# Optimization experiments

Hardware: AMD Instinct MI355X
Metric: run time of the kernel (lower is better)

The kernel has to match this reference:

```python
import jax, jax.numpy as jnp
import numpy as np
import math

B, N, ND, ED, CD, H = 4, 128, 256, 128, 256, 8
D = ND // H

def _ln(x):
    m = jnp.mean(x, axis=-1, keepdims=True)
    v = jnp.mean((x - m) ** 2, axis=-1, keepdims=True)
    return (x - m) / jnp.sqrt(v + 1e-5)

def _lrelu(x):
    return jax.nn.leaky_relu(x, negative_slope=0.1)

def setup_inputs() -> dict:
    key = jax.random.key(0)
    ks = jax.random.split(key, 16)
    rn = lambda k, s: jax.random.normal(k, s, jnp.float32) * 0.02
    return {
        "nodes": jax.random.normal(ks[0], (B, N, ND), jnp.float32),
        "edges": jax.random.normal(ks[1], (B, N, N, ED), jnp.float32),
        "conds": jax.random.normal(ks[2], (B, 1, CD), jnp.float32),
        "Wc": rn(ks[3], (CD, 4 * ND)), "bc": jnp.zeros((4 * ND,), jnp.float32),
        "Wqkv": rn(ks[4], (ND, 3 * ND)), "bqkv": jnp.zeros((3 * ND,), jnp.float32),
        "Wss": rn(ks[5], (ED, 2 * ND)), "bss": jnp.zeros((2 * ND,), jnp.float32),
        "Wno": rn(ks[6], (ND, ND)), "bno": jnp.zeros((ND,), jnp.float32),
        "Weo": rn(ks[7], (ND, ED)), "beo": jnp.zeros((ED,), jnp.float32),
        "Wn1": rn(ks[8], (ND, 4 * ND)), "bn1": jnp.zeros((4 * ND,), jnp.float32),
        "Wn2": rn(ks[9], (4 * ND, ND)), "bn2": jnp.zeros((ND,), jnp.float32),
        "We1": rn(ks[10], (ED, ED)), "be1": jnp.zeros((ED,), jnp.float32),
        "We2": rn(ks[11], (ED, ED)), "be2": jnp.zeros((ED,), jnp.float32),
    }

def reference(nodes, edges, conds, Wc, bc, Wqkv, bqkv, Wss, bss, Wno, bno, Weo, beo, Wn1, bn1, Wn2, bn2, We1, be1, We2, be2):
    b, n, _ = nodes.shape
    # FiLM conditioning (4 chunks, torch chunk order)
    cond = conds @ Wc + bc  # (b,1,4*ND)
    mul_in, add_in, mul_out, add_out = jnp.split(cond, 4, axis=-1)
    n_in = _lrelu(_ln(nodes) * (1.0 + mul_in) + add_in)
    e_in = _lrelu(_ln(edges))
    # attention
    qkv = n_in @ Wqkv + bqkv
    q, k, v = jnp.split(qkv, 3, axis=-1)
    q = q.reshape(b, n, H, D).transpose(0, 2, 1, 3)  # (b,h,n,d)
    k = k.reshape(b, n, H, D).transpose(0, 2, 1, 3)
    v = v.reshape(b, n, H, D).transpose(0, 2, 1, 3)
    # outer-product attention tensor (b,h,q,k,d)
    attn5 = q[:, :, :, None, :] * k[:, :, None, :, :]
    ss = e_in @ Wss + bss  # (b,n,n,2*ND)
    shift, scale = jnp.split(ss, 2, axis=-1)
    shift = shift.reshape(b, n, n, H, D).transpose(0, 3, 1, 2, 4)
    scale = scale.reshape(b, n, n, H, D).transpose(0, 3, 1, 2, 4)
    new_e = attn5 * scale + attn5 + shift  # (b,h,q,k,d)
    logits = jnp.sum(new_e, axis=4) / math.sqrt(D)  # (b,h,q,k)
    attn = jax.nn.softmax(logits, axis=2)  # softmax over dim=2 as in source
    # weighted values -> (b,n,H*D), matching values.view/transpose/flatten layout
    wv = jnp.einsum('bhqk,bhkd->bqhd', attn, v).reshape(b, n, ND)
    new_edges = new_e.transpose(0, 2, 3, 1, 4).reshape(b, n, n, ND)
    delta_nodes = wv @ Wno + bno
    delta_edges = _lrelu(new_edges) @ Weo + beo
    nodes = nodes + delta_nodes
    edges = edges + delta_edges
    # FiLM-normed MLP blocks
    n_out = _lrelu(_ln(nodes) * (1.0 + mul_out) + add_out)
    nodes = nodes + (_lrelu(n_out @ Wn1 + bn1) @ Wn2 + bn2)
    e_out = _lrelu(_ln(edges))
    edges = edges + (_lrelu(e_out @ We1 + be1) @ We2 + be2)
    return (nodes, edges)
```

## Files before the change

### kernel.cpp

```cpp
#include <hip/hip_runtime.h>
#include <hip/hip_bf16.h>

#define BB 4
#define NN 128
#define NH 8

typedef __attribute__((ext_vector_type(8))) short short8;
typedef __attribute__((ext_vector_type(4))) float f32x4;

__device__ __forceinline__ float lrelu(float x){ return fmaxf(x, 0.1f*x); }
__device__ __forceinline__ unsigned short f2b(float x){
  __hip_bfloat16 h = __float2bfloat16(x);
  return *reinterpret_cast<unsigned short*>(&h);
}
__device__ __forceinline__ short8 ldf(const unsigned short* p){ return *(const short8*)p; }


__global__ __launch_bounds__(256) void k_setup(
    const float* Wss, const float* Weo, const float* We1, const float* We2,
    const float* Wqkv, const float* Wno, const float* Wn1, const float* Wn2,
    const float* conds, const float* Wc, const float* bc,
    unsigned short* wbf, float* cond){
  __shared__ float tile[32][33];
  __shared__ float c[256];
  int bid = blockIdx.x, t = threadIdx.x;
  if (bid < 896){
    const float* src; int K, N; size_t doff; int tid;
    if      (bid < 64)  { src=Wss;  K=128;  N=512;  doff=0;      tid=bid; }
    else if (bid < 96)  { src=Weo;  K=256;  N=128;  doff=65536;  tid=bid-64; }
    else if (bid < 112) { src=We1;  K=128;  N=128;  doff=98304;  tid=bid-96; }
    else if (bid < 128) { src=We2;  K=128;  N=128;  doff=114688; tid=bid-112; }
    else if (bid < 320) { src=Wqkv; K=256;  N=768;  doff=131072; tid=bid-128; }
    else if (bid < 384) { src=Wno;  K=256;  N=256;  doff=327680; tid=bid-320; }
    else if (bid < 640) { src=Wn1;  K=256;  N=1024; doff=393216; tid=bid-384; }
    else                { src=Wn2;  K=1024; N=256;  doff=655360; tid=bid-640; }
    int ntk = K >> 5;
    int k0 = (tid % ntk) * 32, n0 = (tid / ntk) * 32;
    int r = t >> 3, c4 = (t & 7) * 4;
    float4 v = *(const float4*)(src + (size_t)(k0+r)*N + n0 + c4);
    tile[r][c4+0]=v.x; tile[r][c4+1]=v.y; tile[r][c4+2]=v.z; tile[r][c4+3]=v.w;
    __syncthreads();
    ushort4 o;
    o.x = f2b(tile[c4+0][r]); o.y = f2b(tile[c4+1][r]);
    o.z = f2b(tile[c4+2][r]); o.w = f2b(tile[c4+3][r]);
    *(ushort4*)(wbf + doff + (size_t)(n0+r)*K + k0 + c4) = o;
  } else {
    int i = bid - 896;
    int b = i >> 2, j = (i&3)*256 + t;
    c[t] = conds[(size_t)b*256 + t];
    __syncthreads();
    float acc = bc[j];
    for (int kk = 0; kk < 256; kk++) acc += c[kk]*Wc[(size_t)kk*1024 + j];
    cond[b*1024 + j] = acc;
  }
}

#define NSTR 260
__global__ __launch_bounds__(256) void k_nodeA(const float* __restrict__ nodes,
    const float* __restrict__ cond, const unsigned short* __restrict__ WqkvT,
    const float* __restrict__ bqkv, float* __restrict__ qbuf,
    float* __restrict__ kT, unsigned short* __restrict__ vT){
  __shared__ float nbuf[16*NSTR];
  __shared__ __align__(16) unsigned short abuf[16*264];
  __shared__ float psum[256], psq[256], mrow[16], irow[16];
  int t = threadIdx.x;
  int rg = blockIdx.x >> 2, slice = blockIdx.x & 3;
  int b = rg >> 3, n0 = (rg & 7)*16;
  int l = t & 63, w = t >> 6, l15 = l & 15, q = l >> 4;

  const float4* src = (const float4*)(nodes + ((size_t)(b*128+n0))*256);
  #pragma unroll
  for (int i = 0; i < 4; i++){
    int f = t + i*256; int r = f >> 6, c4 = f & 63;
    *(float4*)(nbuf + r*NSTR + c4*4) = src[f];
  }
  __syncthreads();
  {
    int r = t >> 4, p = t & 15;
    float s = 0.f, s2 = 0.f;
    #pragma unroll
    for (int i = 0; i < 16; i++){ float v = nbuf[r*NSTR + p + 16*i]; s += v; s2 += v*v; }
    psum[t] = s; psq[t] = s2;
  }
  __syncthreads();
  if (t < 16){
    float s = 0.f, s2 = 0.f;
    #pragma unroll
    for (int i = 0; i < 16; i++){ s += psum[t*16+i]; s2 += psq[t*16+i]; }
    float m = s*(1.f/256);
    mrow[t] = m; irow[t] = rsqrtf(s2*(1.f/256) - m*m + 1e-5f);
  }
  __syncthreads();
  #pragma unroll
  for (int i = 0; i < 16; i++){
    int f = t + i*256; int r = f >> 8, cc = f & 255;
    float x = (nbuf[r*NSTR+cc]-mrow[r])*irow[r]*(1.f+cond[b*1024+cc]) + cond[b*1024+256+cc];
    abuf[r*264+cc] = f2b(lrelu(x));
  }
  __syncthreads();
  short8 af[8];
  #pragma unroll
  for (int k = 0; k < 8; k++) af[k] = ldf(abuf + l15*264 + k*32 + q*8);
  #pragma unroll
  for (int tt = 0; tt < 3; tt++){
    int cc = slice*192 + w*48 + tt*16 + l15;
    const unsigned short* bp = WqkvT + (size_t)cc*256 + q*8;
    f32x4 acc = {0.f,0.f,0.f,0.f};
    #pragma unroll
    for (int k = 0; k < 8; k++) acc = __builtin_amdgcn_mfma_f32_16x16x32_bf16(af[k], ldf(bp + k*32), acc,0,0,0);
    float bb = bqkv[cc];
    if (cc < 256){
      #pragma unroll
      for (int r = 0; r < 4; r++) qbuf[(size_t)(b*128+n0+q*4+r)*256 + cc] = acc[r] + bb;
    } else if (cc < 512){
      float4 kv; kv.x = acc[0]+bb; kv.y = acc[1]+bb; kv.z = acc[2]+bb; kv.w = acc[3]+bb;
      *(float4*)(kT + ((size_t)(b*256 + cc-256))*128 + n0 + q*4) = kv;
    } else {
      ushort4 vv; vv.x = f2b(acc[0]+bb); vv.y = f2b(acc[1]+bb); vv.z = f2b(acc[2]+bb); vv.w = f2b(acc[3]+bb);
      *(ushort4*)(vT + ((size_t)(b*256 + cc-512))*128 + n0 + q*4) = vv;
    }
  }
}

#define ASTR 136
#define LSTR 264
__global__ __launch_bounds__(512) void k_edge(
    const float* __restrict__ edges, const float* __restrict__ qbuf, const float* __restrict__ kT,
    const unsigned short* __restrict__ WssT, const float* __restrict__ bss,
    const unsigned short* __restrict__ WeoT, const float* __restrict__ beo,
    const unsigned short* __restrict__ We1T, const float* __restrict__ be1,
    const unsigned short* __restrict__ We2T, const float* __restrict__ be2,
    float* __restrict__ logitsT, float* __restrict__ out_edges){
  __shared__ __align__(16) unsigned short abuf[32*ASTR];
  __shared__ __align__(16) unsigned short lbuf[32*LSTR];
  __shared__ float qvs[256], lgs[256];
  __shared__ float redS[32][8], redQ[32][8], mrow[32], irow[32];

  int t = threadIdx.x;
  int p0 = blockIdx.x * 32;
  int b  = p0 >> 14, qi = (p0 >> 7) & 127, ki0 = p0 & 127;
  int w = t >> 6, l15 = t & 15, q = (t & 63) >> 4;

  {
    if (t < 256) qvs[t] = qbuf[(size_t)(b*128 + qi)*256 + t];
    const float4* src = (const float4*)(edges + (size_t)p0*128);
    #pragma unroll
    for (int i=0;i<2;i++){
      int idx = t + i*512;
      float4 ev = src[idx];
      int r = idx >> 5, c4 = idx & 31;
      float s  = ev.x + ev.y + ev.z + ev.w;
      float s2 = ev.x*ev.x + ev.y*ev.y + ev.z*ev.z + ev.w*ev.w;
      #pragma unroll
      for (int mm=1; mm<32; mm<<=1){ s += __shfl_xor(s,mm); s2 += __shfl_xor(s2,mm); }
      float m = s*(1.f/128);
      float inv = rsqrtf(s2*(1.f/128) - m*m + 1e-5f);
      ushort4 pk;
      pk.x = f2b(lrelu((ev.x - m)*inv)); pk.y = f2b(lrelu((ev.y - m)*inv));
      pk.z = f2b(lrelu((ev.z - m)*inv)); pk.w = f2b(lrelu((ev.w - m)*inv));
      *(ushort4*)(abuf + r*ASTR + c4*4) = pk;
    }
  }
  __syncthreads();

  const float isd = 0.17677669529663687f;
  {
    short8 af[2][4];
    #pragma unroll
    for (int s=0;s<2;s++)
      #pragma unroll
      for (int k=0;k<4;k++) af[s][k] = ldf(abuf + (s*16+l15)*ASTR + k*32 + q*8);
    float hsPrev[2][4];
    #pragma unroll
    for (int tt=0; tt<2; tt++){
      int cc = w*32 + tt*16 + l15;
      const unsigned short* bsp = WssT + (size_t)cc*128 + q*8;
      const unsigned short* bcp = WssT + (size_t)(cc+256)*128 + q*8;
      f32x4 aS[2], aC[2];
      aS[0]={0.f,0.f,0.f,0.f}; aS[1]=aS[0]; aC[0]=aS[0]; aC[1]=aS[0];
      #pragma unroll
      for (int k=0;k<4;k++){
        short8 b0 = ldf(bsp + k*32);
        short8 b1 = ldf(bcp + k*32);
        aS[0] = __builtin_amdgcn_mfma_f32_16x16x32_bf16(af[0][k], b0, aS[0],0,0,0);
        aS[1] = __builtin_amdgcn_mfma_f32_16x16x32_bf16(af[1][k], b0, aS[1],0,0,0);
        aC[0] = __builtin_amdgcn_mfma_f32_16x16x32_bf16(af[0][k], b1, aC[0],0,0,0);
        aC[1] = __builtin_amdgcn_mfma_f32_16x16x32_bf16(af[1][k], b1, aC[1],0,0,0);
      }
      float bS = bss[cc], bC = bss[256+cc], qv = qvs[cc];
      float hs[2][4];
      #pragma unroll
      for (int s=0;s<2;s++){
        float4 kv4 = *(const float4*)(kT + ((size_t)(b*256+cc))*128 + ki0 + s*16 + q*4);
        float kvv[4] = {kv4.x, kv4.y, kv4.z, kv4.w};
        #pragma unroll
        for (int r=0;r<4;r++){
          int row = s*16 + q*4 + r;
          float ne = qv*kvv[r]*(1.f + aC[s][r] + bC) + aS[s][r] + bS;
          lbuf[row*LSTR + cc] = f2b(lrelu(ne));
          float vv = ne;
          vv += __shfl_xor(vv,1); vv += __shfl_xor(vv,2);
          vv += __shfl_xor(vv,4); vv += __shfl_xor(vv,8);
          hs[s][r] = vv;
        }
      }
      if (tt == 0){
        #pragma unroll
        for (int s=0;s<2;s++)
          #pragma unroll
          for (int r=0;r<4;r++) hsPrev[s][r] = hs[s][r];
      } else if (l15 == 0){
        #pragma unroll
        for (int s=0;s<2;s++)
          #pragma unroll
          for (int r=0;r<4;r++)
            lgs[w*32 + s*16 + q*4 + r] = hsPrev[s][r] + hs[s][r];
      }
    }
  }
  __syncthreads();
  if (t < 256)
    logitsT[((size_t)(b*8 + (t>>5))*128 + ki0 + (t&31))*128 + qi] = lgs[t] * isd;

  float res[2][4];
  int ec = w*16 + l15;
  {
    f32x4 acc0={0.f,0.f,0.f,0.f}, acc1=acc0;
    #pragma unroll
    for (int k=0;k<8;k++){
      short8 lf0 = ldf(lbuf + l15*LSTR + k*32 + q*8);
      short8 lf1 = ldf(lbuf + (16+l15)*LSTR + k*32 + q*8);
      short8 bf = ldf(WeoT + (size_t)ec*256 + k*32 + q*8);
      acc0 = __builtin_amdgcn_mfma_f32_16x16x32_bf16(lf0, bf, acc0,0,0,0);
      acc1 = __builtin_amdgcn_mfma_f32_16x16x32_bf16(lf1, bf, acc1,0,0,0);
    }
    float bb = beo[ec];
    #pragma unroll
    for (int r=0;r<4;r++){
      res[0][r] = edges[(size_t)(p0 + q*4+r)*128 + ec] + acc0[r] + bb;
      res[1][r] = edges[(size_t)(p0 + 16 + q*4+r)*128 + ec] + acc1[r] + bb;
    }
  }
  #pragma unroll
  for (int s=0;s<2;s++)
    #pragma unroll
    for (int r=0;r<4;r++){
      float ps = res[s][r], p2 = res[s][r]*res[s][r];
      ps += __shfl_xor(ps,1); ps += __shfl_xor(ps,2); ps += __shfl_xor(ps,4); ps += __shfl_xor(ps,8);
      p2 += __shfl_xor(p2,1); p2 += __shfl_xor(p2,2); p2 += __shfl_xor(p2,4); p2 += __shfl_xor(p2,8);
      if (l15 == 0){ redS[s*16+q*4+r][w] = ps; redQ[s*16+q*4+r][w] = p2; }
    }
  __syncthreads();
  if (t < 32){
    float s = 0.f, s2 = 0.f;
    #pragma unroll
    for (int i=0;i<8;i++){ s += redS[t][i]; s2 += redQ[t][i]; }
    float m = s*(1.f/128);
    mrow[t] = m; irow[t] = rsqrtf(s2*(1.f/128) - m*m + 1e-5f);
  }
  __syncthreads();
  #pragma unroll
  for (int s=0;s<2;s++)
    #pragma unroll
    for (int r=0;r<4;r++){
      int row = s*16 + q*4 + r;
      abuf[row*ASTR + ec] = f2b(lrelu((res[s][r] - mrow[row])*irow[row]));
    }
  __syncthreads();

  unsigned short* hbuf = lbuf;
  {
    f32x4 acc0={0.f,0.f,0.f,0.f}, acc1=acc0;
    #pragma unroll
    for (int k=0;k<4;k++){
      short8 a0 = ldf(abuf + l15*ASTR + k*32 + q*8);
      short8 a1 = ldf(abuf + (16+l15)*ASTR + k*32 + q*8);
      short8 bf = ldf(We1T + (size_t)ec*128 + k*32 + q*8);
      acc0 = __builtin_amdgcn_mfma_f32_16x16x32_bf16(a0, bf, acc0,0,0,0);
      acc1 = __builtin_amdgcn_mfma_f32_16x16x32_bf16(a1, bf, acc1,0,0,0);
    }
    float bb = be1[ec];
    #pragma unroll
    for (int r=0;r<4;r++){
      hbuf[(q*4+r)*ASTR + ec] = f2b(lrelu(acc0[r] + bb));
      hbuf[(16+q*4+r)*ASTR + ec] = f2b(lrelu(acc1[r] + bb));
    }
  }
  __syncthreads();
  {
    f32x4 acc0={0.f,0.f,0.f,0.f}, acc1=acc0;
    #pragma unroll
    for (int k=0;k<4;k++){
      short8 h0 = ldf(hbuf + l15*ASTR + k*32 + q*8);
      short8 h1 = ldf(hbuf + (16+l15)*ASTR + k*32 + q*8);
      short8 bf = ldf(We2T + (size_t)ec*128 + k*32 + q*8);
      acc0 = __builtin_amdgcn_mfma_f32_16x16x32_bf16(h0, bf, acc0,0,0,0);
      acc1 = __builtin_amdgcn_mfma_f32_16x16x32_bf16(h1, bf, acc1,0,0,0);
    }
    float bb = be2[ec];
    #pragma unroll
    for (int r=0;r<4;r++){
      out_edges[(size_t)(p0 + q*4+r)*128 + ec] = res[0][r] + acc0[r] + bb;
      out_edges[(size_t)(p0 + 16 + q*4+r)*128 + ec] = res[1][r] + acc1[r] + bb;
    }
  }
}

__global__ void k_softmax(const float* __restrict__ logitsT, unsigned short* __restrict__ attnB){
  int t = threadIdx.x, w = t>>6, l = t&63;
  int row = blockIdx.x*4 + w;
  const float* src = logitsT + (size_t)row*128;
  float x0 = src[l], x1 = src[l+64];
  float mx = fmaxf(x0,x1);
  #pragma unroll
  for (int m=1;m<64;m<<=1) mx = fmaxf(mx, __shfl_xor(mx,m));
  float e0 = expf(x0-mx), e1 = expf(x1-mx);
  float s = e0+e1;
  #pragma unroll
  for (int m=1;m<64;m<<=1) s += __shfl_xor(s,m);
  float inv = 1.f/s;
  int bh = row>>7, ki = row&127;
  attnB[((size_t)bh*128 + l)*128 + ki]    = f2b(e0*inv);
  attnB[((size_t)bh*128 + l+64)*128 + ki] = f2b(e1*inv);
}

#define HSTR 1040
__global__ __launch_bounds__(512) void k_node(
    const unsigned short* __restrict__ attnB, const unsigned short* __restrict__ vT,
    const float* __restrict__ nodes, const float* __restrict__ cond,
    const unsigned short* __restrict__ WnoT, const float* __restrict__ bno,
    const unsigned short* __restrict__ Wn1T, const float* __restrict__ bn1,
    const unsigned short* __restrict__ Wn2T, const float* __restrict__ bn2,
    float* __restrict__ out_nodes){
  __shared__ __align__(16) unsigned short abuf[16*264];
  __shared__ __align__(16) unsigned short hbuf[16*HSTR];
  __shared__ float redS[16][8], redQ[16][8], mrow[16], irow[16];
  int t = threadIdx.x;
  int b = blockIdx.x >> 3, n0 = (blockIdx.x & 7)*16;
  int w = t >> 6, l15 = t & 15, q = (t & 63) >> 4;

  {
    const unsigned short* ap = attnB + ((size_t)(b*8+w)*128 + n0 + l15)*128 + q*8;
    short8 af[4];
    #pragma unroll
    for (int k=0;k<4;k++) af[k] = ldf(ap + k*32);
    #pragma unroll
    for (int tt=0;tt<2;tt++){
      int cc = w*32 + tt*16 + l15;
      const unsigned short* bp = vT + (size_t)(b*256+cc)*128 + q*8;
      f32x4 acc = {0.f,0.f,0.f,0.f};
      #pragma unroll
      for (int k=0;k<4;k++) acc = __builtin_amdgcn_mfma_f32_16x16x32_bf16(af[k], ldf(bp + k*32), acc,0,0,0);
      #pragma unroll
      for (int r=0;r<4;r++) abuf[(q*4+r)*264 + cc] = f2b(acc[r]);
    }
  }
  __syncthreads();

  float res[2][4];
  {
    short8 af[8];
    #pragma unroll
    for (int k=0;k<8;k++) af[k] = ldf(abuf + l15*264 + k*32 + q*8);
    #pragma unroll
    for (int tt=0;tt<2;tt++){
      int cc = w*32 + tt*16 + l15;
      const unsigned short* bp = WnoT + (size_t)cc*256 + q*8;
      f32x4 acc = {0.f,0.f,0.f,0.f};
      #pragma unroll
      for (int k=0;k<8;k++) acc = __builtin_amdgcn_mfma_f32_16x16x32_bf16(af[k], ldf(bp + k*32), acc,0,0,0);
      float bb = bno[cc];
      #pragma unroll
      for (int r=0;r<4;r++)
        res[tt][r] = nodes[(size_t)(b*128+n0+q*4+r)*256 + cc] + acc[r] + bb;
    }
  }
  #pragma unroll
  for (int r=0;r<4;r++){
    float ps = res[0][r]+res[1][r];
    float p2 = res[0][r]*res[0][r]+res[1][r]*res[1][r];
    ps += __shfl_xor(ps,1); ps += __shfl_xor(ps,2); ps += __shfl_xor(ps,4); ps += __shfl_xor(ps,8);
    p2 += __shfl_xor(p2,1); p2 += __shfl_xor(p2,2); p2 += __shfl_xor(p2,4); p2 += __shfl_xor(p2,8);
    if (l15 == 0){ redS[q*4+r][w] = ps; redQ[q*4+r][w] = p2; }
  }
  __syncthreads();
  if (t < 16){
    float s = 0.f, s2 = 0.f;
    #pragma unroll
    for (int i=0;i<8;i++){ s += redS[t][i]; s2 += redQ[t][i]; }
    float m = s*(1.f/256);
    mrow[t] = m; irow[t] = rsqrtf(s2*(1.f/256) - m*m + 1e-5f);
  }
  __syncthreads();
  #pragma unroll
  for (int tt=0;tt<2;tt++){
    int cc = w*32 + tt*16 + l15;
    float mul = 1.f + cond[b*1024 + 512 + cc];
    float add = cond[b*1024 + 768 + cc];
    #pragma unroll
    for (int r=0;r<4;r++){
      int row = q*4+r;
      abuf[row*264 + cc] = f2b(lrelu((res[tt][r] - mrow[row])*irow[row]*mul + add));
    }
  }
  __syncthreads();
  {
    short8 af[8];
    #pragma unroll
    for (int k=0;k<8;k++) af[k] = ldf(abuf + l15*264 + k*32 + q*8);
    #pragma unroll
    for (int tt=0;tt<8;tt++){
      int cc = w*128 + tt*16 + l15;
      const unsigned short* bp = Wn1T + (size_t)cc*256 + q*8;
      f32x4 acc = {0.f,0.f,0.f,0.f};
      #pragma unroll
      for (int k=0;k<8;k++) acc = __builtin_amdgcn_mfma_f32_16x16x32_bf16(af[k], ldf(bp + k*32), acc,0,0,0);
      float bb = bn1[cc];
      #pragma unroll
      for (int r=0;r<4;r++)
        hbuf[(q*4+r)*HSTR + cc] = f2b(lrelu(acc[r] + bb));
    }
  }
  __syncthreads();
  {
    f32x4 acc2[2];
    acc2[0]={0.f,0.f,0.f,0.f}; acc2[1]=acc2[0];
    for (int k=0;k<32;k++){
      short8 hf = ldf(hbuf + l15*HSTR + k*32 + q*8);
      #pragma unroll
      for (int tt=0;tt<2;tt++){
        int cc = w*32 + tt*16 + l15;
        short8 bf = ldf(Wn2T + (size_t)cc*1024 + k*32 + q*8);
        acc2[tt] = __builtin_amdgcn_mfma_f32_16x16x32_bf16(hf, bf, acc2[tt],0,0,0);
      }
    }
    #pragma unroll
    for (int tt=0;tt<2;tt++){
      int cc = w*32 + tt*16 + l15;
      float bb = bn2[cc];
      #pragma unroll
      for (int r=0;r<4;r++)
        out_nodes[(size_t)(b*128+n0+q*4+r)*256 + cc] = res[tt][r] + acc2[tt][r] + bb;
    }
  }
}

extern "C" void kernel_launch(void* const* d_in, const int* in_sizes, int n_inp,
                              void* d_out, int out_size, void* d_ws, size_t ws_size,
                              hipStream_t stream){
  const float* nodes = (const float*)d_in[0];
  const float* edges = (const float*)d_in[1];
  const float* conds = (const float*)d_in[2];
  const float* Wc   = (const float*)d_in[3];
  const float* bc   = (const float*)d_in[4];
  const float* Wqkv = (const float*)d_in[5];
  const float* bqkv = (const float*)d_in[6];
  const float* Wss  = (const float*)d_in[7];
  const float* bss  = (const float*)d_in[8];
  const float* Wno  = (const float*)d_in[9];
  const float* bno  = (const float*)d_in[10];
  const float* Weo  = (const float*)d_in[11];
  const float* beo  = (const float*)d_in[12];
  const float* Wn1  = (const float*)d_in[13];
  const float* bn1  = (const float*)d_in[14];
  const float* Wn2  = (const float*)d_in[15];
  const float* bn2  = (const float*)d_in[16];
  const float* We1  = (const float*)d_in[17];
  const float* be1  = (const float*)d_in[18];
  const float* We2  = (const float*)d_in[19];
  const float* be2  = (const float*)d_in[20];

  float* ws      = (float*)d_ws;
  float* cond    = ws;
  float* qbuf    = cond + 4096;
  float* kT      = qbuf + 131072;
  float* logitsT = kT + 131072;
  unsigned short* attnB = (unsigned short*)(logitsT + 524288);
  unsigned short* vT    = attnB + 524288;
  unsigned short* wbf   = vT + 131072;

  unsigned short* WssT  = wbf;
  unsigned short* WeoT  = wbf + 65536;
  unsigned short* We1T  = wbf + 98304;
  unsigned short* We2T  = wbf + 114688;
  unsigned short* WqkvT = wbf + 131072;
  unsigned short* WnoT  = wbf + 327680;
  unsigned short* Wn1T  = wbf + 393216;
  unsigned short* Wn2T  = wbf + 655360;

  float* out_nodes = (float*)d_out;
  float* out_edges = out_nodes + 131072;

  k_setup<<<912, 256, 0, stream>>>(Wss, Weo, We1, We2, Wqkv, Wno, Wn1, Wn2,
                                   conds, Wc, bc, wbf, cond);
  k_nodeA<<<128, 256, 0, stream>>>(nodes, cond, WqkvT, bqkv, qbuf, kT, vT);
  k_edge<<<BB*NN*NN/32, 512, 0, stream>>>(edges, qbuf, kT, WssT, bss, WeoT, beo,
                                          We1T, be1, We2T, be2, logitsT, out_edges);
  k_softmax<<<BB*NH*NN/4, 256, 0, stream>>>(logitsT, attnB);
  k_node<<<32, 512, 0, stream>>>(attnB, vT, nodes, cond, WnoT, bno, Wn1T, bn1,
                                 Wn2T, bn2, out_nodes);
}
```

Before: 260.6 us.

## Halve edge block size, split node MLP into two kernels, rework softmax

The edge kernel now runs 256 threads per block, with each wave covering two heads and doing twice the output tiles, and LDS strides are padded to 144/272. The softmax moves to a per-(b,h) kernel that transposes through shared memory and uses fast exp. The single 32-block node kernel becomes k_nodeB (attention-value, Wno, LN, Wn1 slice, 128 blocks) plus k_nodeC (Wn2, 128 blocks), passing hidden activations through global workspace. The aim is more parallelism in the node stage and better occupancy in the edge stage, at the cost of an extra launch and a workspace round-trip.

```diff
diff --git a/kernel.cpp b/kernel.cpp
--- a/kernel.cpp
+++ b/kernel.cpp
@@ -61,7 +61,7 @@
     const float* __restrict__ bqkv, float* __restrict__ qbuf,
     float* __restrict__ kT, unsigned short* __restrict__ vT){
   __shared__ float nbuf[16*NSTR];
-  __shared__ __align__(16) unsigned short abuf[16*264];
+  __shared__ __align__(16) unsigned short abuf[16*272];
   __shared__ float psum[256], psq[256], mrow[16], irow[16];
   int t = threadIdx.x;
   int rg = blockIdx.x >> 2, slice = blockIdx.x & 3;
@@ -95,12 +95,12 @@
   for (int i = 0; i < 16; i++){
     int f = t + i*256; int r = f >> 8, cc = f & 255;
     float x = (nbuf[r*NSTR+cc]-mrow[r])*irow[r]*(1.f+cond[b*1024+cc]) + cond[b*1024+256+cc];
-    abuf[r*264+cc] = f2b(lrelu(x));
+    abuf[r*272+cc] = f2b(lrelu(x));
   }
   __syncthreads();
   short8 af[8];
   #pragma unroll
-  for (int k = 0; k < 8; k++) af[k] = ldf(abuf + l15*264 + k*32 + q*8);
+  for (int k = 0; k < 8; k++) af[k] = ldf(abuf + l15*272 + k*32 + q*8);
   #pragma unroll
   for (int tt = 0; tt < 3; tt++){
     int cc = slice*192 + w*48 + tt*16 + l15;
@@ -122,9 +122,9 @@
   }
 }
 
-#define ASTR 136
-#define LSTR 264
-__global__ __launch_bounds__(512) void k_edge(
+#define ASTR 144
+#define LSTR 272
+__global__ __launch_bounds__(256) void k_edge(
     const float* __restrict__ edges, const float* __restrict__ qbuf, const float* __restrict__ kT,
     const unsigned short* __restrict__ WssT, const float* __restrict__ bss,
     const unsigned short* __restrict__ WeoT, const float* __restrict__ beo,
@@ -133,8 +133,8 @@
     float* __restrict__ logitsT, float* __restrict__ out_edges){
   __shared__ __align__(16) unsigned short abuf[32*ASTR];
   __shared__ __align__(16) unsigned short lbuf[32*LSTR];
-  __shared__ float qvs[256], lgs[256];
-  __shared__ float redS[32][8], redQ[32][8], mrow[32], irow[32];
+  __shared__ float qvs[256];
+  __shared__ float redS[32][4], redQ[32][4], mrow[32], irow[32];
 
   int t = threadIdx.x;
   int p0 = blockIdx.x * 32;
@@ -142,11 +142,11 @@
   int w = t >> 6, l15 = t & 15, q = (t & 63) >> 4;
 
   {
-    if (t < 256) qvs[t] = qbuf[(size_t)(b*128 + qi)*256 + t];
+    qvs[t] = qbuf[(size_t)(b*128 + qi)*256 + t];
     const float4* src = (const float4*)(edges + (size_t)p0*128);
     #pragma unroll
-    for (int i=0;i<2;i++){
-      int idx = t + i*512;
+    for (int i=0;i<4;i++){
+      int idx = t + i*256;
       float4 ev = src[idx];
       int r = idx >> 5, c4 = idx & 31;
       float s  = ev.x + ev.y + ev.z + ev.w;
@@ -170,205 +170,254 @@
     for (int s=0;s<2;s++)
       #pragma unroll
       for (int k=0;k<4;k++) af[s][k] = ldf(abuf + (s*16+l15)*ASTR + k*32 + q*8);
-    float hsPrev[2][4];
-    #pragma unroll
-    for (int tt=0; tt<2; tt++){
-      int cc = w*32 + tt*16 + l15;
-      const unsigned short* bsp = WssT + (size_t)cc*128 + q*8;
-      const unsigned short* bcp = WssT + (size_t)(cc+256)*128 + q*8;
-      f32x4 aS[2], aC[2];
-      aS[0]={0.f,0.f,0.f,0.f}; aS[1]=aS[0]; aC[0]=aS[0]; aC[1]=aS[0];
-      #pragma unroll
-      for (int k=0;k<4;k++){
-        short8 b0 = ldf(bsp + k*32);
-        short8 b1 = ldf(bcp + k*32);
-        aS[0] = __builtin_amdgcn_mfma_f32_16x16x32_bf16(af[0][k], b0, aS[0],0,0,0);
-        aS[1] = __builtin_amdgcn_mfma_f32_16x16x32_bf16(af[1][k], b0, aS[1],0,0,0);
-        aC[0] = __builtin_amdgcn_mfma_f32_16x16x32_bf16(af[0][k], b1, aC[0],0,0,0);
-        aC[1] = __builtin_amdgcn_mfma_f32_16x16x32_bf16(af[1][k], b1, aC[1],0,0,0);
-      }
-      float bS = bss[cc], bC = bss[256+cc], qv = qvs[cc];
-      float hs[2][4];
-      #pragma unroll
-      for (int s=0;s<2;s++){
-        float4 kv4 = *(const float4*)(kT + ((size_t)(b*256+cc))*128 + ki0 + s*16 + q*4);
-        float kvv[4] = {kv4.x, kv4.y, kv4.z, kv4.w};
+    #pragma unroll
+    for (int h2=0; h2<2; h2++){
+      int h = w*2 + h2;
+      float ps[2][4] = {{0.f,0.f,0.f,0.f},{0.f,0.f,0.f,0.f}};
+      #pragma unroll
+      for (int tt=0; tt<2; tt++){
+        int cc = h*32 + tt*16 + l15;
+        const unsigned short* bsp = WssT + (size_t)cc*128 + q*8;
+        const unsigned short* bcp = WssT + (size_t)(cc+256)*128 + q*8;
+        f32x4 aS[2], aC[2];
+        aS[0]={0.f,0.f,0.f,0.f}; aS[1]=aS[0]; aC[0]=aS[0]; aC[1]=aS[0];
+        #pragma unroll
+        for (int k=0;k<4;k++){
+          short8 b0 = ldf(bsp + k*32);
+          short8 b1 = ldf(bcp + k*32);
+          aS[0] = __builtin_amdgcn_mfma_f32_16x16x32_bf16(af[0][k], b0, aS[0],0,0,0);
+          aS[1] = __builtin_amdgcn_mfma_f32_16x16x32_bf16(af[1][k], b0, aS[1],0,0,0);
+          aC[0] = __builtin_amdgcn_mfma_f32_16x16x32_bf16(af[0][k], b1, aC[0],0,0,0);
+          aC[1] = __builtin_amdgcn_mfma_f32_16x16x32_bf16(af[1][k], b1, aC[1],0,0,0);
+        }
+        float bS = bss[cc], bC = bss[256+cc], qv = qvs[cc];
+        #pragma unroll
+        for (int s=0;s<2;s++){
+          float4 kv4 = *(const float4*)(kT + ((size_t)(b*256+cc))*128 + ki0 + s*16 + q*4);
+          float kvv[4] = {kv4.x, kv4.y, kv4.z, kv4.w};
+          #pragma unroll
+          for (int r=0;r<4;r++){
+            int row = s*16 + q*4 + r;
+            float ne = qv*kvv[r]*(1.f + aC[s][r] + bC) + aS[s][r] + bS;
+            lbuf[row*LSTR + cc] = f2b(lrelu(ne));
+            ps[s][r] += ne;
+          }
+        }
+      }
+      #pragma unroll
+      for (int s=0;s<2;s++)
+        #pragma unroll
+        for (int r=0;r<4;r++){
+          float v = ps[s][r];
+          v += __shfl_xor(v,1); v += __shfl_xor(v,2);
+          v += __shfl_xor(v,4); v += __shfl_xor(v,8);
+          if (l15 == 0){
+            int ki = ki0 + s*16 + q*4 + r;
+            logitsT[((size_t)(b*8+h)*128 + ki)*128 + qi] = v * isd;
+          }
+        }
+    }
+  }
+  __syncthreads();
+
+  float res[2][2][4];
+  {
+    f32x4 acc[2][2];
+    acc[0][0]={0.f,0.f,0.f,0.f}; acc[0][1]=acc[0][0]; acc[1][0]=acc[0][0]; acc[1][1]=acc[0][0];
+    #pragma unroll
+    for (int k=0;k<8;k++){
+      short8 lf0 = ldf(lbuf + l15*LSTR + k*32 + q*8);
+      short8 lf1 = ldf(lbuf + (16+l15)*LSTR + k*32 + q*8);
+      #pragma unroll
+      for (int tt=0;tt<2;tt++){
+        int ec = w*32 + tt*16 + l15;
+        short8 bf = ldf(WeoT + (size_t)ec*256 + k*32 + q*8);
+        acc[tt][0] = __builtin_amdgcn_mfma_f32_16x16x32_bf16(lf0, bf, acc[tt][0],0,0,0);
+        acc[tt][1] = __builtin_amdgcn_mfma_f32_16x16x32_bf16(lf1, bf, acc[tt][1],0,0,0);
+      }
+    }
+    #pragma unroll
+    for (int tt=0;tt<2;tt++){
+      int ec = w*32 + tt*16 + l15;
+      float bb = beo[ec];
+      #pragma unroll
+      for (int s=0;s<2;s++)
         #pragma unroll
         for (int r=0;r<4;r++){
           int row = s*16 + q*4 + r;
-          float ne = qv*kvv[r]*(1.f + aC[s][r] + bC) + aS[s][r] + bS;
-          lbuf[row*LSTR + cc] = f2b(lrelu(ne));
-          float vv = ne;
-          vv += __shfl_xor(vv,1); vv += __shfl_xor(vv,2);
-          vv += __shfl_xor(vv,4); vv += __shfl_xor(vv,8);
-          hs[s][r] = vv;
+          res[tt][s][r] = edges[(size_t)(p0+row)*128 + ec] + acc[tt][s][r] + bb;
         }
-      }
-      if (tt == 0){
-        #pragma unroll
-        for (int s=0;s<2;s++)
-          #pragma unroll
-          for (int r=0;r<4;r++) hsPrev[s][r] = hs[s][r];
-      } else if (l15 == 0){
-        #pragma unroll
-        for (int s=0;s<2;s++)
-          #pragma unroll
-          for (int r=0;r<4;r++)
-            lgs[w*32 + s*16 + q*4 + r] = hsPrev[s][r] + hs[s][r];
-      }
-    }
-  }
-  __syncthreads();
-  if (t < 256)
-    logitsT[((size_t)(b*8 + (t>>5))*128 + ki0 + (t&31))*128 + qi] = lgs[t] * isd;
-
-  float res[2][4];
-  int ec = w*16 + l15;
-  {
-    f32x4 acc0={0.f,0.f,0.f,0.f}, acc1=acc0;
-    #pragma unroll
-    for (int k=0;k<8;k++){
-      short8 lf0 = ldf(lbuf + l15*LSTR + k*32 + q*8);
-      short8 lf1 = ldf(lbuf + (16+l15)*LSTR + k*32 + q*8);
-      short8 bf = ldf(WeoT + (size_t)ec*256 + k*32 + q*8);
-      acc0 = __builtin_amdgcn_mfma_f32_16x16x32_bf16(lf0, bf, acc0,0,0,0);
-      acc1 = __builtin_amdgcn_mfma_f32_16x16x32_bf16(lf1, bf, acc1,0,0,0);
-    }
-    float bb = beo[ec];
+    }
+  }
+  #pragma unroll
+  for (int s=0;s<2;s++)
     #pragma unroll
     for (int r=0;r<4;r++){
-      res[0][r] = edges[(size_t)(p0 + q*4+r)*128 + ec] + acc0[r] + bb;
-      res[1][r] = edges[(size_t)(p0 + 16 + q*4+r)*128 + ec] + acc1[r] + bb;
-    }
-  }
-  #pragma unroll
-  for (int s=0;s<2;s++)
-    #pragma unroll
-    for (int r=0;r<4;r++){
-      float ps = res[s][r], p2 = res[s][r]*res[s][r];
+      float ps = res[0][s][r] + res[1][s][r];
+      float p2 = res[0][s][r]*res[0][s][r] + res[1][s][r]*res[1][s][r];
       ps += __shfl_xor(ps,1); ps += __shfl_xor(ps,2); ps += __shfl_xor(ps,4); ps += __shfl_xor(ps,8);
       p2 += __shfl_xor(p2,1); p2 += __shfl_xor(p2,2); p2 += __shfl_xor(p2,4); p2 += __shfl_xor(p2,8);
       if (l15 == 0){ redS[s*16+q*4+r][w] = ps; redQ[s*16+q*4+r][w] = p2; }
     }
   __syncthreads();
   if (t < 32){
-    float s = 0.f, s2 = 0.f;
-    #pragma unroll
-    for (int i=0;i<8;i++){ s += redS[t][i]; s2 += redQ[t][i]; }
+    float s = redS[t][0]+redS[t][1]+redS[t][2]+redS[t][3];
+    float s2 = redQ[t][0]+redQ[t][1]+redQ[t][2]+redQ[t][3];
     float m = s*(1.f/128);
     mrow[t] = m; irow[t] = rsqrtf(s2*(1.f/128) - m*m + 1e-5f);
   }
   __syncthreads();
   #pragma unroll
-  for (int s=0;s<2;s++)
-    #pragma unroll
-    for (int r=0;r<4;r++){
-      int row = s*16 + q*4 + r;
-      abuf[row*ASTR + ec] = f2b(lrelu((res[s][r] - mrow[row])*irow[row]));
-    }
+  for (int tt=0;tt<2;tt++){
+    int ec = w*32 + tt*16 + l15;
+    #pragma unroll
+    for (int s=0;s<2;s++)
+      #pragma unroll
+      for (int r=0;r<4;r++){
+        int row = s*16 + q*4 + r;
+        abuf[row*ASTR + ec] = f2b(lrelu((res[tt][s][r] - mrow[row])*irow[row]));
+      }
+  }
   __syncthreads();
 
   unsigned short* hbuf = lbuf;
   {
-    f32x4 acc0={0.f,0.f,0.f,0.f}, acc1=acc0;
+    f32x4 acc[2][2];
+    acc[0][0]={0.f,0.f,0.f,0.f}; acc[0][1]=acc[0][0]; acc[1][0]=acc[0][0]; acc[1][1]=acc[0][0];
     #pragma unroll
     for (int k=0;k<4;k++){
       short8 a0 = ldf(abuf + l15*ASTR + k*32 + q*8);
       short8 a1 = ldf(abuf + (16+l15)*ASTR + k*32 + q*8);
-      short8 bf = ldf(We1T + (size_t)ec*128 + k*32 + q*8);
-      acc0 = __builtin_amdgcn_mfma_f32_16x16x32_bf16(a0, bf, acc0,0,0,0);
-      acc1 = __builtin_amdgcn_mfma_f32_16x16x32_bf16(a1, bf, acc1,0,0,0);
-    }
-    float bb = be1[ec];
-    #pragma unroll
-    for (int r=0;r<4;r++){
-      hbuf[(q*4+r)*ASTR + ec] = f2b(lrelu(acc0[r] + bb));
-      hbuf[(16+q*4+r)*ASTR + ec] = f2b(lrelu(acc1[r] + bb));
-    }
-  }
-  __syncthreads();
-  {
-    f32x4 acc0={0.f,0.f,0.f,0.f}, acc1=acc0;
+      #pragma unroll
+      for (int tt=0;tt<2;tt++){
+        int ec = w*32 + tt*16 + l15;
+        short8 bf = ldf(We1T + (size_t)ec*128 + k*32 + q*8);
+        acc[tt][0] = __builtin_amdgcn_mfma_f32_16x16x32_bf16(a0, bf, acc[tt][0],0,0,0);
+        acc[tt][1] = __builtin_amdgcn_mfma_f32_16x16x32_bf16(a1, bf, acc[tt][1],0,0,0);
+      }
+    }
+    #pragma unroll
+    for (int tt=0;tt<2;tt++){
+      int ec = w*32 + tt*16 + l15;
+      float bb = be1[ec];
+      #pragma unroll
+      for (int r=0;r<4;r++){
+        hbuf[(q*4+r)*ASTR + ec] = f2b(lrelu(acc[tt][0][r] + bb));
+        hbuf[(16+q*4+r)*ASTR + ec] = f2b(lrelu(acc[tt][1][r] + bb));
+      }
+    }
+  }
+  __syncthreads();
+  {
+    f32x4 acc[2][2];
+    acc[0][0]={0.f,0.f,0.f,0.f}; acc[0][1]=acc[0][0]; acc[1][0]=acc[0][0]; acc[1][1]=acc[0][0];
     #pragma unroll
     for (int k=0;k<4;k++){
       short8 h0 = ldf(hbuf + l15*ASTR + k*32 + q*8);
       short8 h1 = ldf(hbuf + (16+l15)*ASTR + k*32 + q*8);
-      short8 bf = ldf(We2T + (size_t)ec*128 + k*32 + q*8);
-      acc0 = __builtin_amdgcn_mfma_f32_16x16x32_bf16(h0, bf, acc0,0,0,0);
-      acc1 = __builtin_amdgcn_mfma_f32_16x16x32_bf16(h1, bf, acc1,0,0,0);
-    }
-    float bb = be2[ec];
-    #pragma unroll
-    for (int r=0;r<4;r++){
-      out_edges[(size_t)(p0 + q*4+r)*128 + ec] = res[0][r] + acc0[r] + bb;
-      out_edges[(size_t)(p0 + 16 + q*4+r)*128 + ec] = res[1][r] + acc1[r] + bb;
-    }
-  }
-}
-
-__global__ void k_softmax(const float* __restrict__ logitsT, unsigned short* __restrict__ attnB){
-  int t = threadIdx.x, w = t>>6, l = t&63;
-  int row = blockIdx.x*4 + w;
-  const float* src = logitsT + (size_t)row*128;
-  float x0 = src[l], x1 = src[l+64];
-  float mx = fmaxf(x0,x1);
-  #pragma unroll
-  for (int m=1;m<64;m<<=1) mx = fmaxf(mx, __shfl_xor(mx,m));
-  float e0 = expf(x0-mx), e1 = expf(x1-mx);
-  float s = e0+e1;
-  #pragma unroll
-  for (int m=1;m<64;m<<=1) s += __shfl_xor(s,m);
-  float inv = 1.f/s;
-  int bh = row>>7, ki = row&127;
-  attnB[((size_t)bh*128 + l)*128 + ki]    = f2b(e0*inv);
-  attnB[((size_t)bh*128 + l+64)*128 + ki] = f2b(e1*inv);
-}
-
-#define HSTR 1040
-__global__ __launch_bounds__(512) void k_node(
+      #pragma unroll
+      for (int tt=0;tt<2;tt++){
+        int ec = w*32 + tt*16 + l15;
+        short8 bf = ldf(We2T + (size_t)ec*128 + k*32 + q*8);
+        acc[tt][0] = __builtin_amdgcn_mfma_f32_16x16x32_bf16(h0, bf, acc[tt][0],0,0,0);
+        acc[tt][1] = __builtin_amdgcn_mfma_f32_16x16x32_bf16(h1, bf, acc[tt][1],0,0,0);
+      }
+    }
+    #pragma unroll
+    for (int tt=0;tt<2;tt++){
+      int ec = w*32 + tt*16 + l15;
+      float bb = be2[ec];
+      #pragma unroll
+      for (int r=0;r<4;r++){
+        out_edges[(size_t)(p0 + q*4+r)*128 + ec] = res[tt][0][r] + acc[tt][0][r] + bb;
+        out_edges[(size_t)(p0 + 16 + q*4+r)*128 + ec] = res[tt][1][r] + acc[tt][1][r] + bb;
+      }
+    }
+  }
+}
+
+__global__ __launch_bounds__(256) void k_attn(const float* __restrict__ logitsT,
+                                              unsigned short* __restrict__ attnB){
+  __shared__ float tile[32][129];
+  __shared__ float mS[128], sS[128];
+  int t = threadIdx.x, w = t >> 6, l = t & 63;
+  const float* base = logitsT + (size_t)blockIdx.x * 16384;
+  for (int i = 0; i < 32; i++){
+    int ki = w*32 + i;
+    float x0 = base[ki*128 + l], x1 = base[ki*128 + 64 + l];
+    float mx = fmaxf(x0, x1);
+    #pragma unroll
+    for (int m=1;m<64;m<<=1) mx = fmaxf(mx, __shfl_xor(mx,m));
+    float s = __expf(x0-mx) + __expf(x1-mx);
+    #pragma unroll
+    for (int m=1;m<64;m<<=1) s += __shfl_xor(s,m);
+    if (l == 0){ mS[ki] = mx; sS[ki] = 1.f/s; }
+  }
+  __syncthreads();
+  unsigned short* obase = attnB + (size_t)blockIdx.x * 16384;
+  for (int c = 0; c < 4; c++){
+    int q0 = c*32;
+    #pragma unroll
+    for (int i = 0; i < 16; i++){
+      int idx = t + i*256; int ki = idx >> 5, qq = idx & 31;
+      tile[qq][ki] = base[ki*128 + q0 + qq];
+    }
+    __syncthreads();
+    #pragma unroll
+    for (int i = 0; i < 16; i++){
+      int idx = t + i*256; int qq = idx >> 7, ki = idx & 127;
+      obase[(q0+qq)*128 + ki] = f2b(__expf(tile[qq][ki] - mS[ki]) * sS[ki]);
+    }
+    __syncthreads();
+  }
+}
+
+#define AB 272
+__global__ __launch_bounds__(256) void k_nodeB(
     const unsigned short* __restrict__ attnB, const unsigned short* __restrict__ vT,
     const float* __restrict__ nodes, const float* __restrict__ cond,
     const unsigned short* __restrict__ WnoT, const float* __restrict__ bno,
     const unsigned short* __restrict__ Wn1T, const float* __restrict__ bn1,
-    const unsigned short* __restrict__ Wn2T, const float* __restrict__ bn2,
-    float* __restrict__ out_nodes){
-  __shared__ __align__(16) unsigned short abuf[16*264];
-  __shared__ __align__(16) unsigned short hbuf[16*HSTR];
-  __shared__ float redS[16][8], redQ[16][8], mrow[16], irow[16];
+    float* __restrict__ nodes1ws, unsigned short* __restrict__ hiddenB){
+  __shared__ __align__(16) unsigned short abuf[16*AB];
+  __shared__ float redS[16][4], redQ[16][4], mrow[16], irow[16];
   int t = threadIdx.x;
-  int b = blockIdx.x >> 3, n0 = (blockIdx.x & 7)*16;
+  int rg = blockIdx.x >> 2, slice = blockIdx.x & 3;
+  int b = rg >> 3, n0 = (rg & 7)*16;
   int w = t >> 6, l15 = t & 15, q = (t & 63) >> 4;
 
-  {
-    const unsigned short* ap = attnB + ((size_t)(b*8+w)*128 + n0 + l15)*128 + q*8;
+  #pragma unroll
+  for (int h2=0; h2<2; h2++){
+    int h = w*2 + h2;
+    const unsigned short* ap = attnB + ((size_t)(b*8+h)*128 + n0 + l15)*128 + q*8;
     short8 af[4];
     #pragma unroll
     for (int k=0;k<4;k++) af[k] = ldf(ap + k*32);
     #pragma unroll
     for (int tt=0;tt<2;tt++){
-      int cc = w*32 + tt*16 + l15;
+      int cc = h*32 + tt*16 + l15;
       const unsigned short* bp = vT + (size_t)(b*256+cc)*128 + q*8;
       f32x4 acc = {0.f,0.f,0.f,0.f};
       #pragma unroll
       for (int k=0;k<4;k++) acc = __builtin_amdgcn_mfma_f32_16x16x32_bf16(af[k], ldf(bp + k*32), acc,0,0,0);
       #pragma unroll
-      for (int r=0;r<4;r++) abuf[(q*4+r)*264 + cc] = f2b(acc[r]);
-    }
-  }
-  __syncthreads();
-
-  float res[2][4];
-  {
-    short8 af[8];
-    #pragma unroll
-    for (int k=0;k<8;k++) af[k] = ldf(abuf + l15*264 + k*32 + q*8);
-    #pragma unroll
-    for (int tt=0;tt<2;tt++){
-      int cc = w*32 + tt*16 + l15;
+      for (int r=0;r<4;r++) abuf[(q*4+r)*AB + cc] = f2b(acc[r]);
+    }
+  }
+  __syncthreads();
+
+  float res[4][4];
+  {
+    short8 aw[8];
+    #pragma unroll
+    for (int k=0;k<8;k++) aw[k] = ldf(abuf + l15*AB + k*32 + q*8);
+    #pragma unroll
+    for (int tt=0;tt<4;tt++){
+      int cc = w*64 + tt*16 + l15;
       const unsigned short* bp = WnoT + (size_t)cc*256 + q*8;
       f32x4 acc = {0.f,0.f,0.f,0.f};
       #pragma unroll
-      for (int k=0;k<8;k++) acc = __builtin_amdgcn_mfma_f32_16x16x32_bf16(af[k], ldf(bp + k*32), acc,0,0,0);
+      for (int k=0;k<8;k++) acc = __builtin_amdgcn_mfma_f32_16x16x32_bf16(aw[k], ldf(bp + k*32), acc,0,0,0);
       float bb = bno[cc];
       #pragma unroll
       for (int r=0;r<4;r++)
@@ -377,71 +426,79 @@
   }
   #pragma unroll
   for (int r=0;r<4;r++){
-    float ps = res[0][r]+res[1][r];
-    float p2 = res[0][r]*res[0][r]+res[1][r]*res[1][r];
+    float ps = res[0][r]+res[1][r]+res[2][r]+res[3][r];
+    float p2 = res[0][r]*res[0][r]+res[1][r]*res[1][r]+res[2][r]*res[2][r]+res[3][r]*res[3][r];
     ps += __shfl_xor(ps,1); ps += __shfl_xor(ps,2); ps += __shfl_xor(ps,4); ps += __shfl_xor(ps,8);
     p2 += __shfl_xor(p2,1); p2 += __shfl_xor(p2,2); p2 += __shfl_xor(p2,4); p2 += __shfl_xor(p2,8);
     if (l15 == 0){ redS[q*4+r][w] = ps; redQ[q*4+r][w] = p2; }
   }
   __syncthreads();
   if (t < 16){
-    float s = 0.f, s2 = 0.f;
-    #pragma unroll
-    for (int i=0;i<8;i++){ s += redS[t][i]; s2 += redQ[t][i]; }
+    float s = redS[t][0]+redS[t][1]+redS[t][2]+redS[t][3];
+    float s2 = redQ[t][0]+redQ[t][1]+redQ[t][2]+redQ[t][3];
     float m = s*(1.f/256);
     mrow[t] = m; irow[t] = rsqrtf(s2*(1.f/256) - m*m + 1e-5f);
   }
   __syncthreads();
   #pragma unroll
-  for (int tt=0;tt<2;tt++){
-    int cc = w*32 + tt*16 + l15;
+  for (int tt=0;tt<4;tt++){
+    int cc = w*64 + tt*16 + l15;
     float mul = 1.f + cond[b*1024 + 512 + cc];
     float add = cond[b*1024 + 768 + cc];
     #pragma unroll
     for (int r=0;r<4;r++){
       int row = q*4+r;
-      abuf[row*264 + cc] = f2b(lrelu((res[tt][r] - mrow[row])*irow[row]*mul + add));
-    }
-  }
-  __syncthreads();
-  {
-    short8 af[8];
-    #pragma unroll
-    for (int k=0;k<8;k++) af[k] = ldf(abuf + l15*264 + k*32 + q*8);
-    #pragma unroll
-    for (int tt=0;tt<8;tt++){
-      int cc = w*128 + tt*16 + l15;
+      abuf[row*AB + cc] = f2b(lrelu((res[tt][r] - mrow[row])*irow[row]*mul + add));
+    }
+  }
+  if (slice == 0){
+    #pragma unroll
+    for (int tt=0;tt<4;tt++){
+      int cc = w*64 + tt*16 + l15;
+      #pragma unroll
+      for (int r=0;r<4;r++)
+        nodes1ws[(size_t)(rg*16 + q*4+r)*256 + cc] = res[tt][r];
+    }
+  }
+  __syncthreads();
+  {
+    short8 a2[8];
+    #pragma unroll
+    for (int k=0;k<8;k++) a2[k] = ldf(abuf + l15*AB + k*32 + q*8);
+    #pragma unroll
+    for (int tt=0;tt<4;tt++){
+      int cc = slice*256 + w*64 + tt*16 + l15;
       const unsigned short* bp = Wn1T + (size_t)cc*256 + q*8;
       f32x4 acc = {0.f,0.f,0.f,0.f};
       #pragma unroll
-      for (int k=0;k<8;k++) acc = __builtin_amdgcn_mfma_f32_16x16x32_bf16(af[k], ldf(bp + k*32), acc,0,0,0);
+      for (int k=0;k<8;k++) acc = __builtin_amdgcn_mfma_f32_16x16x32_bf16(a2[k], ldf(bp + k*32), acc,0,0,0);
       float bb = bn1[cc];
       #pragma unroll
       for (int r=0;r<4;r++)
-        hbuf[(q*4+r)*HSTR + cc] = f2b(lrelu(acc[r] + bb));
-    }
-  }
-  __syncthreads();
-  {
-    f32x4 acc2[2];
-    acc2[0]={0.f,0.f,0.f,0.f}; acc2[1]=acc2[0];
-    for (int k=0;k<32;k++){
-      short8 hf = ldf(hbuf + l15*HSTR + k*32 + q*8);
-      #pragma unroll
-      for (int tt=0;tt<2;tt++){
-        int cc = w*32 + tt*16 + l15;
-        short8 bf = ldf(Wn2T + (size_t)cc*1024 + k*32 + q*8);
-        acc2[tt] = __builtin_amdgcn_mfma_f32_16x16x32_bf16(hf, bf, acc2[tt],0,0,0);
-      }
-    }
-    #pragma unroll
-    for (int tt=0;tt<2;tt++){
-      int cc = w*32 + tt*16 + l15;
-      float bb = bn2[cc];
-      #pragma unroll
-      for (int r=0;r<4;r++)
-        out_nodes[(size_t)(b*128+n0+q*4+r)*256 + cc] = res[tt][r] + acc2[tt][r] + bb;
-    }
+        hiddenB[((size_t)rg*16 + q*4+r)*1024 + cc] = f2b(lrelu(acc[r] + bb));
+    }
+  }
+}
+
+__global__ __launch_bounds__(256) void k_nodeC(
+    const unsigned short* __restrict__ hiddenB, const float* __restrict__ nodes1ws,
+    const unsigned short* __restrict__ Wn2T, const float* __restrict__ bn2,
+    float* __restrict__ out_nodes){
+  int t = threadIdx.x;
+  int rg = blockIdx.x >> 2, cs = blockIdx.x & 3;
+  int w = t >> 6, l15 = t & 15, q = (t & 63) >> 4;
+  int cc = cs*64 + w*16 + l15;
+  const unsigned short* ap = hiddenB + ((size_t)rg*16 + l15)*1024 + q*8;
+  const unsigned short* bp = Wn2T + (size_t)cc*1024 + q*8;
+  f32x4 acc = {0.f,0.f,0.f,0.f};
+  #pragma unroll
+  for (int k=0;k<32;k++)
+    acc = __builtin_amdgcn_mfma_f32_16x16x32_bf16(ldf(ap + k*32), ldf(bp + k*32), acc,0,0,0);
+  float bb = bn2[cc];
+  #pragma unroll
+  for (int r=0;r<4;r++){
+    size_t row = (size_t)rg*16 + q*4 + r;
+    out_nodes[row*256 + cc] = nodes1ws[row*256 + cc] + acc[r] + bb;
   }
 }
 
@@ -470,14 +527,16 @@
   const float* We2  = (const float*)d_in[19];
   const float* be2  = (const float*)d_in[20];
 
-  float* ws      = (float*)d_ws;
-  float* cond    = ws;
-  float* qbuf    = cond + 4096;
-  float* kT      = qbuf + 131072;
-  float* logitsT = kT + 131072;
-  unsigned short* attnB = (unsigned short*)(logitsT + 524288);
-  unsigned short* vT    = attnB + 524288;
-  unsigned short* wbf   = vT + 131072;
+  float* ws       = (float*)d_ws;
+  float* cond     = ws;
+  float* qbuf     = cond + 4096;
+  float* kT       = qbuf + 131072;
+  float* logitsT  = kT + 131072;
+  float* nodes1ws = logitsT + 524288;
+  unsigned short* attnB   = (unsigned short*)(nodes1ws + 131072);
+  unsigned short* vT      = attnB + 524288;
+  unsigned short* hiddenB = vT + 131072;
+  unsigned short* wbf     = hiddenB + 524288;
 
   unsigned short* WssT  = wbf;
   unsigned short* WeoT  = wbf + 65536;
@@ -494,9 +553,10 @@
   k_setup<<<912, 256, 0, stream>>>(Wss, Weo, We1, We2, Wqkv, Wno, Wn1, Wn2,
                                    conds, Wc, bc, wbf, cond);
   k_nodeA<<<128, 256, 0, stream>>>(nodes, cond, WqkvT, bqkv, qbuf, kT, vT);
-  k_edge<<<BB*NN*NN/32, 512, 0, stream>>>(edges, qbuf, kT, WssT, bss, WeoT, beo,
+  k_edge<<<BB*NN*NN/32, 256, 0, stream>>>(edges, qbuf, kT, WssT, bss, WeoT, beo,
                                           We1T, be1, We2T, be2, logitsT, out_edges);
-  k_softmax<<<BB*NH*NN/4, 256, 0, stream>>>(logitsT, attnB);
-  k_node<<<32, 512, 0, stream>>>(attnB, vT, nodes, cond, WnoT, bno, Wn1T, bn1,
-                                 Wn2T, bn2, out_nodes);
-}
+  k_attn<<<BB*NH, 256, 0, stream>>>(logitsT, attnB);
+  k_nodeB<<<128, 256, 0, stream>>>(attnB, vT, nodes, cond, WnoT, bno, Wn1T, bn1,
+                                   nodes1ws, hiddenB);
+  k_nodeC<<<128, 256, 0, stream>>>(hiddenB, nodes1ws, Wn2T, bn2, out_nodes);
+}
```

After: 257.3 us. About the same (-1.3%).
